# Kernel tuning notes

Hardware: AMD Instinct MI355X
Metric: run time of the kernel (lower is better)

The kernel has to match this reference:

```python
import jax, jax.numpy as jnp
import numpy as np

B, S, D = 4, 4096, 1024

def setup_inputs() -> dict:
    key = jax.random.key(0)
    k1, k2, k3 = jax.random.split(key, 3)
    x = jax.random.normal(k1, (B, S, D), dtype=jnp.float32)
    # torch nn.Linear weights: [out_features, in_features], scaled for sanity
    W_qkv = jax.random.normal(k2, (3 * D, D), dtype=jnp.float32) * (1.0 / np.sqrt(D))
    W_o = jax.random.normal(k3, (D, D), dtype=jnp.float32) * (1.0 / np.sqrt(D))
    return {"x": x, "W_qkv": W_qkv, "W_o": W_o}


def reference(x, W_qkv, W_o):
    d_model = x.shape[-1]
    # torch Linear: y = x @ W.T
    qkv = jnp.einsum("bsd,ed->bse", x, W_qkv)  # [B, S, 3D]
    Q, K, V = jnp.split(qkv, 3, axis=-1)
    scale = 1.0 / jnp.sqrt(jnp.asarray(d_model, dtype=x.dtype))
    logits = jnp.einsum("bqd,bkd->bqk", Q, K) * scale  # [B, S, S]
    weights = jax.nn.softmax(logits, axis=-1)
    attn = jnp.einsum("bqk,bkd->bqd", weights, V)  # [B, S, D]
    out = jnp.einsum("bsd,ed->bse", attn, W_o)  # [B, S, D]
    return out
```

## Files before the change

kernel.cpp:

```cpp
#include <hip/hip_runtime.h>
#include <hip/hip_bf16.h>
#include <stdint.h>

typedef unsigned short u16;
typedef __bf16 bf16x8 __attribute__((ext_vector_type(8)));
typedef unsigned short u16x8 __attribute__((ext_vector_type(8)));
typedef float f32x4 __attribute__((ext_vector_type(4)));

__device__ __forceinline__ float bf2f(u16 h) {
  union { uint32_t u; float f; } x;
  x.u = ((uint32_t)h) << 16;
  return x.f;
}
__device__ __forceinline__ u16 f2bf(float f) {
  union { float f; uint32_t u; } x;
  x.f = f;
  uint32_t r = x.u + 0x7FFFu + ((x.u >> 16) & 1u);
  return (u16)(r >> 16);
}

__device__ __forceinline__ void gload_lds16(const u16* g, u16* l) {
  __builtin_amdgcn_global_load_lds(
      (const __attribute__((address_space(1))) uint32_t*)g,
      (__attribute__((address_space(3))) uint32_t*)l, 16, 0, 0);
}

__global__ __launch_bounds__(256) void cvt_all(
    const float* __restrict__ x, const float* __restrict__ w1,
    const float* __restrict__ w2, u16* __restrict__ xb,
    u16* __restrict__ w1b, u16* __restrict__ w2b, int n1, int n2, int n3) {
  int i = blockIdx.x * 256 + threadIdx.x;
  const float* src;
  u16* dst;
  int j = i;
  if (i < n1) { src = x; dst = xb; }
  else if (i < n1 + n2) { src = w1; dst = w1b; j = i - n1; }
  else if (i < n1 + n2 + n3) { src = w2; dst = w2b; j = i - n1 - n2; }
  else return;
  const float4* p = (const float4*)src + (size_t)j * 2;
  float4 a = p[0], b = p[1];
  u16x8 o;
  o[0] = f2bf(a.x); o[1] = f2bf(a.y); o[2] = f2bf(a.z); o[3] = f2bf(a.w);
  o[4] = f2bf(b.x); o[5] = f2bf(b.y); o[6] = f2bf(b.z); o[7] = f2bf(b.w);
  ((u16x8*)dst)[j] = o;
}

template <typename OT, int EPI>
__global__ __launch_bounds__(256) void gemm_bt(
    const u16* __restrict__ A, int lda, long zsA,
    const u16* __restrict__ B, int ldb, long zsB,
    OT* __restrict__ C, int ldc, long zsC,
    int K, float scale, const float* __restrict__ rs) {
  const int z = blockIdx.z;
  A += (long)z * zsA;
  B += (long)z * zsB;
  C += (long)z * zsC;
  if constexpr (EPI == 2) rs += (long)z * 4096;

  __shared__ __align__(16) u16 As[2 * 128 * 32];
  __shared__ __align__(16) u16 Bs[2 * 128 * 32];
  const int tid  = threadIdx.x;
  const int m0   = blockIdx.y * 128;
  const int n0   = blockIdx.x * 128;
  const int wave = tid >> 6;
  const int lane = tid & 63;
  const int wm   = (wave >> 1) * 64;
  const int wn   = (wave & 1) * 64;
  const int l15  = lane & 15;
  const int quad = lane >> 4;

  f32x4 acc[4][4];
#pragma unroll
  for (int i = 0; i < 4; ++i)
#pragma unroll
    for (int j = 0; j < 4; ++j) acc[i][j] = f32x4{0.f, 0.f, 0.f, 0.f};

  const u16* gA0 = A + (size_t)(m0 + (tid >> 2)) * lda + (tid & 3) * 8;
  const u16* gA1 = A + (size_t)(m0 + 64 + (tid >> 2)) * lda + (tid & 3) * 8;
  const u16* gB0 = B + (size_t)(n0 + (tid >> 2)) * ldb + (tid & 3) * 8;
  const u16* gB1 = B + (size_t)(n0 + 64 + (tid >> 2)) * ldb + (tid & 3) * 8;
  u16* lA0 = As + tid * 8;
  u16* lA1 = As + (256 + tid) * 8;
  u16* lB0 = Bs + tid * 8;
  u16* lB1 = Bs + (256 + tid) * 8;

  for (int k0 = 0; k0 < K; k0 += 64) {
    __syncthreads();
#pragma unroll
    for (int s = 0; s < 2; ++s) {
      gload_lds16(gA0 + k0 + s * 32, lA0 + s * 4096);
      gload_lds16(gA1 + k0 + s * 32, lA1 + s * 4096);
      gload_lds16(gB0 + k0 + s * 32, lB0 + s * 4096);
      gload_lds16(gB1 + k0 + s * 32, lB1 + s * 4096);
    }
    __syncthreads();

#pragma unroll
    for (int s = 0; s < 2; ++s) {
      u16x8 a[4], b[4];
#pragma unroll
      for (int i = 0; i < 4; ++i)
        a[i] = *(const u16x8*)(As + s * 4096 + (wm + i * 16 + l15) * 32 + quad * 8);
#pragma unroll
      for (int j = 0; j < 4; ++j)
        b[j] = *(const u16x8*)(Bs + s * 4096 + (wn + j * 16 + l15) * 32 + quad * 8);
#pragma unroll
      for (int i = 0; i < 4; ++i)
#pragma unroll
        for (int j = 0; j < 4; ++j)
          acc[i][j] = __builtin_amdgcn_mfma_f32_16x16x32_bf16(
              __builtin_bit_cast(bf16x8, a[i]), __builtin_bit_cast(bf16x8, b[j]),
              acc[i][j], 0, 0, 0);
    }
  }

#pragma unroll
  for (int i = 0; i < 4; ++i) {
#pragma unroll
    for (int r = 0; r < 4; ++r) {
      const int row = m0 + wm + i * 16 + quad * 4 + r;
      float mul = scale;
      if constexpr (EPI == 2) mul = scale / rs[row];
      const size_t ro = (size_t)row * ldc;
#pragma unroll
      for (int j = 0; j < 4; ++j) {
        float v = acc[i][j][r] * mul;
        if constexpr (EPI == 1) v = __expf(v);
        const int col = n0 + wn + j * 16 + l15;
        if constexpr (__is_same(OT, float))
          C[ro + col] = v;
        else
          C[ro + col] = f2bf(v);
      }
    }
  }
}

__global__ __launch_bounds__(256) void rowsum_rows(
    const u16* __restrict__ P, long zsP, float* __restrict__ rs) {
  const int row = blockIdx.x;
  const int z   = blockIdx.y;
  const u16* p = P + (long)z * zsP + (size_t)row * 4096;
  const int tid  = threadIdx.x;
  const int lane = tid & 63;
  const int wave = tid >> 6;

  u16x8 h0 = *(const u16x8*)(p + tid * 16);
  u16x8 h1 = *(const u16x8*)(p + tid * 16 + 8);
  float s = 0.f;
#pragma unroll
  for (int j = 0; j < 8; ++j) s += bf2f(h0[j]) + bf2f(h1[j]);
  for (int o = 32; o > 0; o >>= 1) s += __shfl_xor(s, o, 64);
  __shared__ float red[4];
  if (lane == 0) red[wave] = s;
  __syncthreads();
  if (tid == 0) rs[(size_t)z * 4096 + row] = red[0] + red[1] + red[2] + red[3];
}

__global__ __launch_bounds__(256) void transpose_v(
    const u16* __restrict__ V, int ldv, long zsV,
    u16* __restrict__ Vt, int ldt, long zsT) {
  const int z = blockIdx.z;
  V  += (long)z * zsV;
  Vt += (long)z * zsT;
  __shared__ u16 T[64][65];
  const int d0 = blockIdx.x * 64;
  const int s0 = blockIdx.y * 64;
  const int tid = threadIdx.x;
  const int c = tid & 63;
  const int rbase = (tid >> 6) * 16;
#pragma unroll
  for (int r = 0; r < 16; ++r)
    T[rbase + r][c] = V[(size_t)(s0 + rbase + r) * ldv + d0 + c];
  __syncthreads();
#pragma unroll
  for (int r = 0; r < 16; ++r)
    Vt[(size_t)(d0 + rbase + r) * ldt + s0 + c] = T[c][rbase + r];
}

extern "C" void kernel_launch(void* const* d_in, const int* in_sizes, int n_in,
                              void* d_out, int out_size, void* d_ws, size_t ws_size,
                              hipStream_t stream) {
  const float* x    = (const float*)d_in[0];
  const float* Wqkv = (const float*)d_in[1];
  const float* Wo   = (const float*)d_in[2];
  float* out = (float*)d_out;

  const int Bn = 4, S = 4096, D = 1024;
  const int M = Bn * S;
  const int E = 3 * D;
  const long SE = (long)S * E, SS = (long)S * S, DS = (long)D * S, SD = (long)S * D;

  const int nz = (ws_size >= (size_t)226492416) ? 2 : 1;

  char* ws = (char*)d_ws;
  size_t off = 0;
  u16* qkv = (u16*)(ws + off);  off += (size_t)M * E * 2;
  u16* Sb  = (u16*)(ws + off);  off += (size_t)nz * S * S * 2;
  u16* Vt  = (u16*)(ws + off);  off += (size_t)nz * D * S * 2;
  u16* xb  = (u16*)(ws + off);  off += (size_t)M * D * 2;
  u16* attn = xb;
  u16* Wqkvb = (u16*)(ws + off); off += (size_t)E * D * 2;
  u16* Wob   = (u16*)(ws + off); off += (size_t)D * D * 2;
  float* rs = (float*)Wqkvb;

  const int n1 = M * D / 8, n2 = E * D / 8, n3 = D * D / 8;
  cvt_all<<<(n1 + n2 + n3 + 255) / 256, 256, 0, stream>>>(
      x, Wqkv, Wo, xb, Wqkvb, Wob, n1, n2, n3);

  gemm_bt<u16, 0><<<dim3(E / 128, M / 128, 1), 256, 0, stream>>>(
      xb, D, 0, Wqkvb, D, 0, qkv, E, 0, D, 1.0f, nullptr);

  const float scl = 0.03125f;
  for (int c = 0; c < Bn; c += nz) {
    const u16* Qc = qkv + (size_t)c * SE;
    transpose_v<<<dim3(D / 64, S / 64, nz), 256, 0, stream>>>(
        Qc + 2 * D, E, SE, Vt, S, DS);
    gemm_bt<u16, 1><<<dim3(S / 128, S / 128, nz), 256, 0, stream>>>(
        Qc, E, SE, Qc + D, E, SE, Sb, S, SS, D, scl, nullptr);
    rowsum_rows<<<dim3(S, nz), 256, 0, stream>>>(Sb, SS, rs);
    gemm_bt<u16, 2><<<dim3(D / 128, S / 128, nz), 256, 0, stream>>>(
        Sb, S, SS, Vt, S, DS, attn + (size_t)c * SD, D, SD, S, 1.0f, rs);
  }

  gemm_bt<float, 0><<<dim3(D / 128, M / 128, 1), 256, 0, stream>>>(
      attn, D, 0, Wob, D, 0, out, D, 0, D, 1.0f, nullptr);
}
```

Measured before the change: 679.1 us.

## Add 256x256 pipelined GEMM with swizzled LDS and interleaved async loads

```diff
diff --git a/kernel.cpp b/kernel.cpp
--- a/kernel.cpp
+++ b/kernel.cpp
@@ -136,6 +136,150 @@
   }
 }
 
+#define BAR() __builtin_amdgcn_s_barrier()
+#define PRIO(n) __builtin_amdgcn_s_setprio(n)
+#define WAITV(n) asm volatile("s_waitcnt vmcnt(" #n ")" ::: "memory")
+
+#define STG(c, h, q, t)                                                         \
+  gload_lds16(((h) < 2 ? gAs : gBs) +                                           \
+                  (size_t)(((h) & 1) * 128 + (q) * 64) * ((h) < 2 ? lda : ldb) + \
+                  (size_t)(t) * 64,                                             \
+              lds + (c) * 32768 + ((h) < 2 ? 0 : 16384) +                       \
+                  (((h) & 1) * 8 + (q) * 4) * 1024 + wsub * 512)
+
+#define LDA_Q(c, qm)                                                            \
+  {                                                                             \
+    _Pragma("unroll") for (int ii = 0; ii < 4; ++ii) {                          \
+      _Pragma("unroll") for (int kk = 0; kk < 2; ++kk)                          \
+          a[(qm) * 4 + ii][kk] = *(const u16x8*)(lds + (c) * 32768 +            \
+              ((wm8 + (qm) * 4 + ii) * 2 + kk) * 512 + rq);                     \
+    }                                                                           \
+  }
+
+#define LDB_Q(c, qn)                                                            \
+  {                                                                             \
+    _Pragma("unroll") for (int jj = 0; jj < 2; ++jj) {                          \
+      _Pragma("unroll") for (int kk = 0; kk < 2; ++kk)                          \
+          b[(qn) * 2 + jj][kk] = *(const u16x8*)(lds + (c) * 32768 + 16384 +    \
+              ((wn4 + (qn) * 2 + jj) * 2 + kk) * 512 + rq);                     \
+    }                                                                           \
+  }
+
+#define MFMA_Q(qm, qn)                                                          \
+  {                                                                             \
+    PRIO(1);                                                                    \
+    _Pragma("unroll") for (int kk = 0; kk < 2; ++kk) {                          \
+      _Pragma("unroll") for (int ii = 0; ii < 4; ++ii) {                        \
+        _Pragma("unroll") for (int jj = 0; jj < 2; ++jj)                        \
+            acc[(qm) * 4 + ii][(qn) * 2 + jj] =                                 \
+                __builtin_amdgcn_mfma_f32_16x16x32_bf16(                        \
+                    __builtin_bit_cast(bf16x8, a[(qm) * 4 + ii][kk]),           \
+                    __builtin_bit_cast(bf16x8, b[(qn) * 2 + jj][kk]),           \
+                    acc[(qm) * 4 + ii][(qn) * 2 + jj], 0, 0, 0);                \
+      }                                                                         \
+    }                                                                           \
+    PRIO(0);                                                                    \
+  }
+
+template <typename OT, int EPI>
+__global__ __launch_bounds__(512, 2) void gemm256(
+    const u16* __restrict__ A, int lda, long zsA,
+    const u16* __restrict__ B, int ldb, long zsB,
+    OT* __restrict__ C, int ldc, long zsC,
+    int K, float scale, const float* __restrict__ rs) {
+  __shared__ __align__(16) u16 lds[65536];
+  const int z = blockIdx.z;
+  A += (long)z * zsA;
+  B += (long)z * zsB;
+  C += (long)z * zsC;
+  if constexpr (EPI == 2) rs += (long)z * 4096;
+
+  const int tid  = threadIdx.x;
+  const int lane = tid & 63;
+  const int w    = tid >> 6;
+  const int wm   = w >> 2;
+  const int wn   = w & 3;
+  const int wm8  = wm * 8;
+  const int wn4  = wn * 4;
+  const int l15  = lane & 15;
+  const int quad = lane >> 4;
+  const int m0   = blockIdx.y * 256;
+  const int n0   = blockIdx.x * 256;
+
+  const int srow = (w >> 1) * 16 + (lane >> 2);
+  const int kcol = ((lane & 3) * 8) ^ ((lane & 32) ? 16 : 0);
+  const int skb  = w & 1;
+  const u16* gAs = A + (size_t)(m0 + srow) * lda + skb * 32 + kcol;
+  const u16* gBs = B + (size_t)(n0 + srow) * ldb + skb * 32 + kcol;
+  const int wsub = (w >> 1) * 2 + skb;
+
+  const int rq = (l15 * 32 + quad * 8) ^ ((l15 & 8) << 1);
+
+  f32x4 acc[8][4];
+#pragma unroll
+  for (int i = 0; i < 8; ++i)
+#pragma unroll
+    for (int j = 0; j < 4; ++j) acc[i][j] = f32x4{0.f, 0.f, 0.f, 0.f};
+  u16x8 a[8][2], b[4][2];
+
+  const int ni = K >> 7;
+
+#pragma unroll
+  for (int h = 0; h < 4; ++h) { STG(0, h, 0, 0); STG(0, h, 1, 0); }
+  STG(1, 0, 0, 1); STG(1, 0, 1, 1);
+  STG(1, 1, 0, 1); STG(1, 1, 1, 1);
+  WAITV(4);
+  BAR();
+
+  for (int i = 0; i < ni; ++i) {
+    const int t1 = 2 * i + 1, t2 = 2 * i + 2, t3 = 2 * i + 3;
+    const bool more = (i + 1 < ni);
+
+    LDA_Q(0, 0); LDB_Q(0, 0);
+    STG(1, 2, 0, t1); STG(1, 2, 1, t1);
+    BAR(); MFMA_Q(0, 0); BAR();
+    LDA_Q(0, 1); LDB_Q(0, 1);
+    STG(1, 3, 0, t1); STG(1, 3, 1, t1);
+    BAR(); MFMA_Q(0, 1); BAR();
+    if (more) { STG(0, 0, 0, t2); STG(0, 0, 1, t2); }
+    BAR(); MFMA_Q(1, 0); BAR();
+    if (more) { STG(0, 1, 0, t2); STG(0, 1, 1, t2); WAITV(4); }
+    else { WAITV(0); }
+    BAR(); MFMA_Q(1, 1); BAR();
+    LDA_Q(1, 0); LDB_Q(1, 0);
+    if (more) { STG(0, 2, 0, t2); STG(0, 2, 1, t2); }
+    BAR(); MFMA_Q(0, 0); BAR();
+    LDA_Q(1, 1); LDB_Q(1, 1);
+    if (more) { STG(0, 3, 0, t2); STG(0, 3, 1, t2); }
+    BAR(); MFMA_Q(0, 1); BAR();
+    if (more) { STG(1, 0, 0, t3); STG(1, 0, 1, t3); }
+    BAR(); MFMA_Q(1, 0); BAR();
+    if (more) { STG(1, 1, 0, t3); STG(1, 1, 1, t3); WAITV(4); }
+    BAR(); MFMA_Q(1, 1); BAR();
+  }
+
+#pragma unroll
+  for (int i = 0; i < 8; ++i) {
+#pragma unroll
+    for (int r = 0; r < 4; ++r) {
+      const int row = m0 + wm * 128 + i * 16 + quad * 4 + r;
+      float mul = scale;
+      if constexpr (EPI == 2) mul = scale / rs[row];
+      const size_t ro = (size_t)row * ldc;
+#pragma unroll
+      for (int j = 0; j < 4; ++j) {
+        float v = acc[i][j][r] * mul;
+        if constexpr (EPI == 1) v = __expf(v);
+        const int col = n0 + wn * 64 + j * 16 + l15;
+        if constexpr (__is_same(OT, float))
+          C[ro + col] = v;
+        else
+          C[ro + col] = f2bf(v);
+      }
+    }
+  }
+}
+
 __global__ __launch_bounds__(256) void rowsum_rows(
     const u16* __restrict__ P, long zsP, float* __restrict__ rs) {
   const int row = blockIdx.x;
@@ -208,7 +352,7 @@
   cvt_all<<<(n1 + n2 + n3 + 255) / 256, 256, 0, stream>>>(
       x, Wqkv, Wo, xb, Wqkvb, Wob, n1, n2, n3);
 
-  gemm_bt<u16, 0><<<dim3(E / 128, M / 128, 1), 256, 0, stream>>>(
+  gemm256<u16, 0><<<dim3(E / 256, M / 256, 1), 512, 0, stream>>>(
       xb, D, 0, Wqkvb, D, 0, qkv, E, 0, D, 1.0f, nullptr);
 
   const float scl = 0.03125f;
@@ -216,13 +360,13 @@
     const u16* Qc = qkv + (size_t)c * SE;
     transpose_v<<<dim3(D / 64, S / 64, nz), 256, 0, stream>>>(
         Qc + 2 * D, E, SE, Vt, S, DS);
-    gemm_bt<u16, 1><<<dim3(S / 128, S / 128, nz), 256, 0, stream>>>(
+    gemm256<u16, 1><<<dim3(S / 256, S / 256, nz), 512, 0, stream>>>(
         Qc, E, SE, Qc + D, E, SE, Sb, S, SS, D, scl, nullptr);
     rowsum_rows<<<dim3(S, nz), 256, 0, stream>>>(Sb, SS, rs);
     gemm_bt<u16, 2><<<dim3(D / 128, S / 128, nz), 256, 0, stream>>>(
         Sb, S, SS, Vt, S, DS, attn + (size_t)c * SD, D, SD, S, 1.0f, rs);
   }
 
-  gemm_bt<float, 0><<<dim3(D / 128, M / 128, 1), 256, 0, stream>>>(
+  gemm256<float, 0><<<dim3(D / 256, M / 256, 1), 512, 0, stream>>>(
       attn, D, 0, Wob, D, 0, out, D, 0, D, 1.0f, nullptr);
 }
```

Measured after the change: 665.6 us. 1.02x faster.
